# Performance work log

Hardware: AMD Instinct MI355X
Metric: run time of the kernel (lower is better)

## Reference

```python
import jax, jax.numpy as jnp
import numpy as np

MARGIN = 0.3
N, D, NUM_CLASSES = 384, 128, 16


def setup_inputs() -> dict:
    key = jax.random.key(0)
    k1, k2 = jax.random.split(key)
    embeddings = jax.random.normal(k1, (N, D), dtype=jnp.float32)
    labels = jax.random.randint(k2, (N,), 0, NUM_CLASSES, dtype=jnp.int32)
    return {"embeddings": embeddings, "labels": labels}


def reference(embeddings, labels):
    # pairwise squared-euclidean distance matrix [N, N]
    sq = jnp.sum(embeddings * embeddings, axis=1)
    dist = sq[:, None] + sq[None, :] - 2.0 * (embeddings @ embeddings.T)

    # same[i, j] == True iff labels match (anchor-positive pairs; includes i==j,
    # matching the original which keeps the diagonal of `ap`)
    same = labels[:, None] == labels[None, :]  # [N, N]

    # triplet loss L[i, p, n] = d(i,p) - d(i,n) + margin  (vectorized per-class loop)
    L = dist[:, :, None] - dist[:, None, :] + MARGIN  # [N, N, N]
    valid = same[:, :, None] & (~same)[:, None, :]    # p positive, n negative
    mask = valid & (L > 0.0) & (L < MARGIN)

    losses = jnp.sum(jnp.where(mask, L, 0.0))
    count = jnp.sum(mask).astype(jnp.float32)
    return losses, count
```

## Files before the change

kernel.cpp:

```cpp
#include <hip/hip_runtime.h>

#define NN 384
#define DD 128
#define MARGIN 0.3f
#define BLOCK 384

__global__ __launch_bounds__(BLOCK) void triplet_kernel(
    const float* __restrict__ emb, const int* __restrict__ labels,
    float* __restrict__ out)
{
    __shared__ float4 ei4[DD / 4];
    __shared__ float dist_row[NN];
    __shared__ int labels_s[NN];
    __shared__ unsigned char same[NN];
    __shared__ short pos_list[NN];
    __shared__ int npos;
    __shared__ float red_l[BLOCK / 64];
    __shared__ float red_c[BLOCK / 64];

    const int i = blockIdx.x;
    const int tid = threadIdx.x;

    labels_s[tid] = labels[tid];
    if (tid == 0) npos = 0;
    if (tid < DD / 4) {
        ei4[tid] = ((const float4*)emb)[i * (DD / 4) + tid];
    }
    __syncthreads();

    const int li = labels_s[i];

    {
        const float4* ej = ((const float4*)emb) + tid * (DD / 4);
        float acc = 0.f;
#pragma unroll 8
        for (int d = 0; d < DD / 4; ++d) {
            float4 a = ei4[d];
            float4 b = ej[d];
            float dx = a.x - b.x;
            float dy = a.y - b.y;
            float dz = a.z - b.z;
            float dw = a.w - b.w;
            acc += dx * dx + dy * dy + dz * dz + dw * dw;
        }
        dist_row[tid] = acc;
        bool s = (labels_s[tid] == li);
        same[tid] = s ? 1 : 0;
        if (s) {
            int idx = atomicAdd(&npos, 1);
            pos_list[idx] = (short)tid;
        }
    }
    __syncthreads();

    float loss = 0.f;
    float cnt = 0.f;
    {
        const bool is_neg = (same[tid] == 0);
        const float dn = dist_row[tid];
        const int np = npos;
        for (int pi = 0; pi < np; ++pi) {
            const float dp = dist_row[pos_list[pi]];
            const float L = dp - dn + MARGIN;
            if (is_neg & (L > 0.f) & (L < MARGIN)) {
                loss += L;
                cnt += 1.f;
            }
        }
    }

    for (int off = 32; off > 0; off >>= 1) {
        loss += __shfl_down(loss, off, 64);
        cnt  += __shfl_down(cnt, off, 64);
    }
    const int wave = tid >> 6;
    const int lane = tid & 63;
    if (lane == 0) {
        red_l[wave] = loss;
        red_c[wave] = cnt;
    }
    __syncthreads();
    if (tid == 0) {
        float Lb = 0.f, Cb = 0.f;
#pragma unroll
        for (int w = 0; w < BLOCK / 64; ++w) { Lb += red_l[w]; Cb += red_c[w]; }
        atomicAdd(&out[0], Lb);
        atomicAdd(&out[1], Cb);
    }
}

extern "C" void kernel_launch(void* const* d_in, const int* in_sizes, int n_in,
                              void* d_out, int out_size, void* d_ws, size_t ws_size,
                              hipStream_t stream) {
    const float* emb = (const float*)d_in[0];
    const int* labels = (const int*)d_in[1];
    float* out = (float*)d_out;

    triplet_kernel<<<NN, BLOCK, 0, stream>>>(emb, labels, out);
}
```

Measured before the change: 70.54 us.

## Process four anchors per block to reuse embedding row loads

Each block now handles four anchor rows instead of one, so every thread's global embedding row is loaded once and reused for four distance computations, and the grid shrinks to a quarter. This cuts redundant global/L2 traffic on the embedding matrix and amortizes block setup and the final atomics. In exchange there are only 96 blocks on a device with many CUs, so parallelism drops and per-block serial work in the triplet loop grows fourfold.

Result: faster. 68.70 us (-2.6%).

```diff
diff --git a/kernel.cpp b/kernel.cpp
--- a/kernel.cpp
+++ b/kernel.cpp
@@ -4,63 +4,73 @@
 #define DD 128
 #define MARGIN 0.3f
 #define BLOCK 384
+#define ANCH 4
 
 __global__ __launch_bounds__(BLOCK) void triplet_kernel(
     const float* __restrict__ emb, const int* __restrict__ labels,
     float* __restrict__ out)
 {
-    __shared__ float4 ei4[DD / 4];
-    __shared__ float dist_row[NN];
+    __shared__ float4 ei4[ANCH][DD / 4];
+    __shared__ float dist_row[ANCH][NN];
     __shared__ int labels_s[NN];
-    __shared__ unsigned char same[NN];
-    __shared__ short pos_list[NN];
-    __shared__ int npos;
+    __shared__ short pos_list[ANCH][NN];
+    __shared__ int npos[ANCH];
     __shared__ float red_l[BLOCK / 64];
     __shared__ float red_c[BLOCK / 64];
 
-    const int i = blockIdx.x;
     const int tid = threadIdx.x;
+    const int i0 = blockIdx.x * ANCH;
 
     labels_s[tid] = labels[tid];
-    if (tid == 0) npos = 0;
-    if (tid < DD / 4) {
-        ei4[tid] = ((const float4*)emb)[i * (DD / 4) + tid];
+    if (tid < ANCH) npos[tid] = 0;
+    if (tid < ANCH * (DD / 4)) {
+        int a = tid >> 5;
+        int d = tid & 31;
+        ei4[a][d] = ((const float4*)emb)[(i0 + a) * (DD / 4) + d];
     }
     __syncthreads();
 
-    const int li = labels_s[i];
+    int la[ANCH];
+#pragma unroll
+    for (int a = 0; a < ANCH; ++a) la[a] = labels_s[i0 + a];
+    const int lj = labels_s[tid];
 
     {
         const float4* ej = ((const float4*)emb) + tid * (DD / 4);
-        float acc = 0.f;
-#pragma unroll 8
+        float acc[ANCH] = {0.f, 0.f, 0.f, 0.f};
+#pragma unroll 4
         for (int d = 0; d < DD / 4; ++d) {
-            float4 a = ei4[d];
             float4 b = ej[d];
-            float dx = a.x - b.x;
-            float dy = a.y - b.y;
-            float dz = a.z - b.z;
-            float dw = a.w - b.w;
-            acc += dx * dx + dy * dy + dz * dz + dw * dw;
+#pragma unroll
+            for (int a = 0; a < ANCH; ++a) {
+                float4 av = ei4[a][d];
+                float dx = av.x - b.x;
+                float dy = av.y - b.y;
+                float dz = av.z - b.z;
+                float dw = av.w - b.w;
+                acc[a] += dx * dx + dy * dy + dz * dz + dw * dw;
+            }
         }
-        dist_row[tid] = acc;
-        bool s = (labels_s[tid] == li);
-        same[tid] = s ? 1 : 0;
-        if (s) {
-            int idx = atomicAdd(&npos, 1);
-            pos_list[idx] = (short)tid;
+#pragma unroll
+        for (int a = 0; a < ANCH; ++a) {
+            dist_row[a][tid] = acc[a];
+            if (lj == la[a]) {
+                int idx = atomicAdd(&npos[a], 1);
+                pos_list[a][idx] = (short)tid;
+            }
         }
     }
     __syncthreads();
 
     float loss = 0.f;
     float cnt = 0.f;
-    {
-        const bool is_neg = (same[tid] == 0);
-        const float dn = dist_row[tid];
-        const int np = npos;
+#pragma unroll
+    for (int a = 0; a < ANCH; ++a) {
+        const bool is_neg = (lj != la[a]);
+        const float dn = dist_row[a][tid];
+        const int np = npos[a];
         for (int pi = 0; pi < np; ++pi) {
-            const float dp = dist_row[pos_list[pi]];
+            const float dp = dist_row[a][pos_list[a][pi]];
             const float L = dp - dn + MARGIN;
             if (is_neg & (L > 0.f) & (L < MARGIN)) {
                 loss += L;
@@ -96,5 +106,5 @@
     const int* labels = (const int*)d_in[1];
     float* out = (float*)d_out;
 
-    triplet_kernel<<<NN, BLOCK, 0, stream>>>(emb, labels, out);
+    triplet_kernel<<<NN / ANCH, BLOCK, 0, stream>>>(emb, labels, out);
 }
```
